# Performance work log

Measured on AMD Instinct MI355X. Metric: run time of the kernel, lower is better.

The kernel has to match this reference:

```python
import jax, jax.numpy as jnp
import numpy as np

B, S, D = 8, 2048, 256
H, HD = 4, 64  # num_heads, head_size; H*HD == D


def setup_inputs() -> dict:
    key = jax.random.key(0)
    ks = jax.random.split(key, 9)
    scale = 0.02
    return {
        "x": jax.random.normal(ks[0], (B, S, D), dtype=jnp.float32),
        "Wq": jax.random.normal(ks[1], (D, H * HD), dtype=jnp.float32) * scale,
        "bq": jnp.zeros((H * HD,), dtype=jnp.float32),
        "Wk": jax.random.normal(ks[2], (D, H * HD), dtype=jnp.float32) * scale,
        "bk": jnp.zeros((H * HD,), dtype=jnp.float32),
        "Wv": jax.random.normal(ks[3], (D, H * HD), dtype=jnp.float32) * scale,
        "bv": jnp.zeros((H * HD,), dtype=jnp.float32),
        "Wo": jax.random.normal(ks[4], (H * HD, D), dtype=jnp.float32) * scale,
        "bo": jnp.zeros((D,), dtype=jnp.float32),
    }


def _split_heads(t):
    # [B, S, H*HD] -> [B, H, S, HD]
    b, s, _ = t.shape
    return t.reshape(b, s, H, HD).transpose(0, 2, 1, 3)


def reference(x, Wq, bq, Wk, bk, Wv, bv, Wo, bo):
    q = _split_heads(x @ Wq + bq)
    k = _split_heads(x @ Wk + bk)
    v = _split_heads(x @ Wv + bv)
    scores = jnp.einsum("bhqd,bhkd->bhqk", q, k) / jnp.sqrt(jnp.float32(HD))
    weights = jax.nn.softmax(scores, axis=-1)
    attn = jnp.einsum("bhqk,bhkd->bhqd", weights, v)  # [B, H, S, HD]
    concat = attn.transpose(0, 2, 1, 3).reshape(x.shape[0], -1, H * HD)
    return concat @ Wo + bo
```

## Files before the change

### kernel.cpp

```cpp
#include <hip/hip_runtime.h>
#include <hip/hip_bf16.h>

namespace {

constexpr int B_ = 8, S = 2048, D = 256, H = 4, HD = 64;
constexpr int M = B_ * S;

typedef __attribute__((ext_vector_type(8))) short bf16x8;
typedef __attribute__((ext_vector_type(4))) short bf16x4;
typedef __attribute__((ext_vector_type(4))) float f32x4;
typedef __attribute__((ext_vector_type(16))) float f32x16;
typedef __attribute__((ext_vector_type(4))) unsigned uint4v;

__device__ inline short f2bf(float x) {
  __hip_bfloat16 h = __float2bfloat16(x);
  short s;
  __builtin_memcpy(&s, &h, 2);
  return s;
}

__device__ inline f32x4 mfma16(bf16x8 a, bf16x8 b, f32x4 c) {
  return __builtin_amdgcn_mfma_f32_16x16x32_bf16(a, b, c, 0, 0, 0);
}
__device__ inline f32x16 mfma32(bf16x8 a, bf16x8 b, f32x16 c) {
  return __builtin_amdgcn_mfma_f32_32x32x16_bf16(a, b, c, 0, 0, 0);
}

__device__ inline float exp2a(float x) {
  float r;
  asm("v_exp_f32 %0, %1" : "=v"(r) : "v"(x));
  return r;
}

__device__ inline unsigned cvtpk(float lo, float hi) {
  unsigned r;
  asm("v_cvt_pk_bf16_f32 %0, %1, %2" : "=v"(r) : "v"(lo), "v"(hi));
  return r;
}

__device__ inline bf16x4 pk4(float a, float b, float c, float d) {
  unsigned lo = cvtpk(a, b), hi = cvtpk(c, d);
  uint2 u{lo, hi};
  bf16x4 r;
  __builtin_memcpy(&r, &u, 8);
  return r;
}

__device__ inline bf16x8 ld_cvt8(const float* p) {
  float4 a = *(const float4*)p;
  float4 b = *(const float4*)(p + 4);
  uint4v u = {cvtpk(a.x, a.y), cvtpk(a.z, a.w), cvtpk(b.x, b.y), cvtpk(b.z, b.w)};
  bf16x8 r;
  __builtin_memcpy(&r, &u, 16);
  return r;
}

__global__ __launch_bounds__(256) void prep_w_kernel(
    const float* __restrict__ Wq, const float* __restrict__ Wk,
    const float* __restrict__ Wv, const float* __restrict__ Wo,
    short* __restrict__ WqT, short* __restrict__ WkT,
    short* __restrict__ WvT, short* __restrict__ WoT) {
  const int blk = blockIdx.x, t = threadIdx.x;
  const int wq = blk >> 4, n0 = (blk & 15) * 16;
  const float* W = wq == 0 ? Wq : wq == 1 ? Wk : wq == 2 ? Wv : Wo;
  short* Wt = wq == 0 ? WqT : wq == 1 ? WkT : wq == 2 ? WvT : WoT;
#pragma unroll
  for (int j4 = 0; j4 < 4; ++j4) {
    float4 v = *(const float4*)(W + (size_t)t * 256 + n0 + j4 * 4);
    Wt[(n0 + j4 * 4 + 0) * 256 + t] = f2bf(v.x);
    Wt[(n0 + j4 * 4 + 1) * 256 + t] = f2bf(v.y);
    Wt[(n0 + j4 * 4 + 2) * 256 + t] = f2bf(v.z);
    Wt[(n0 + j4 * 4 + 3) * 256 + t] = f2bf(v.w);
  }
}

__global__ __launch_bounds__(256) void gemm_qkv_kernel(
    const float* __restrict__ x,
    const short* __restrict__ WqT, const short* __restrict__ WkT,
    const short* __restrict__ WvT,
    const float* __restrict__ bq, const float* __restrict__ bk,
    const float* __restrict__ bv,
    short* __restrict__ Qo, short* __restrict__ Ko, short* __restrict__ Vt) {
  const int bx = blockIdx.x;
  const int which = blockIdx.y;
  const short* Wt = which == 0 ? WqT : which == 1 ? WkT : WvT;
  const float* bias = which == 0 ? bq : which == 1 ? bk : bv;

  __shared__ short Xs[2][64 * 32];
  __shared__ short Ws[2][256 * 32];

  const int tid = threadIdx.x;
  const int wid = tid >> 6, lane = tid & 63;
  const int l15 = lane & 15, l4 = lane >> 4;
  const int nt0 = wid * 4;

  const float* xsrc = x + ((size_t)(bx * 64 + (tid >> 2))) * 256 + (tid & 3) * 8;
  const short* wsrc = Wt + ((size_t)(tid >> 2)) * 256 + (tid & 3) * 8;
  short* xdst0 = &Xs[0][tid * 8];
  short* xdst1 = &Xs[1][tid * 8];
  short* wdst0 = &Ws[0][tid * 8];
  short* wdst1 = &Ws[1][tid * 8];

  bf16x8 xr, wr[4];
  xr = ld_cvt8(xsrc);
#pragma unroll
  for (int p = 0; p < 4; ++p) wr[p] = *(const bf16x8*)(wsrc + (size_t)p * 64 * 256);
  *(bf16x8*)xdst0 = xr;
#pragma unroll
  for (int p = 0; p < 4; ++p) *(bf16x8*)(wdst0 + p * 2048) = wr[p];
  __syncthreads();

  f32x4 acc[4][4];
#pragma unroll
  for (int i = 0; i < 4; ++i)
#pragma unroll
    for (int mh = 0; mh < 4; ++mh) acc[i][mh] = f32x4{0.f, 0.f, 0.f, 0.f};

  for (int ks = 0; ks < 8; ++ks) {
    const int cur = ks & 1;
    if (ks < 7) {
      xr = ld_cvt8(xsrc + (ks + 1) * 32);
#pragma unroll
      for (int p = 0; p < 4; ++p)
        wr[p] = *(const bf16x8*)(wsrc + (size_t)p * 64 * 256 + (ks + 1) * 32);
    }
    bf16x8 wf[4], xf[4];
#pragma unroll
    for (int i = 0; i < 4; ++i)
      wf[i] = *(const bf16x8*)&Ws[cur][((nt0 + i) * 16 + l15) * 32 + l4 * 8];
#pragma unroll
    for (int mh = 0; mh < 4; ++mh)
      xf[mh] = *(const bf16x8*)&Xs[cur][(mh * 16 + l15) * 32 + l4 * 8];
    if (which == 2) {
#pragma unroll
      for (int i = 0; i < 4; ++i)
#pragma unroll
        for (int mh = 0; mh < 4; ++mh)
          acc[i][mh] = mfma16(xf[mh], wf[i], acc[i][mh]);
    } else {
#pragma unroll
      for (int i = 0; i < 4; ++i)
#pragma unroll
        for (int mh = 0; mh < 4; ++mh)
          acc[i][mh] = mfma16(wf[i], xf[mh], acc[i][mh]);
    }
    if (ks < 7) {
      short* xd = (cur ? xdst0 : xdst1);
      short* wd = (cur ? wdst0 : wdst1);
      *(bf16x8*)xd = xr;
#pragma unroll
      for (int p = 0; p < 4; ++p) *(bf16x8*)(wd + p * 2048) = wr[p];
    }
    __syncthreads();
  }

  if (which == 2) {
    const int m0 = bx * 64 + l4 * 4;
#pragma unroll
    for (int i = 0; i < 4; ++i) {
      const int n = (nt0 + i) * 16 + l15;
      const float bi = bias[n];
      const int h = n >> 6, d = n & 63;
#pragma unroll
      for (int mh = 0; mh < 4; ++mh) {
        const int m = m0 + mh * 16;
        const int bb = m >> 11, s0 = m & 2047;
        bf16x4 r = pk4(acc[i][mh][0] + bi, acc[i][mh][1] + bi,
                       acc[i][mh][2] + bi, acc[i][mh][3] + bi);
        *(bf16x4*)(Vt + (((size_t)bb * H + h) * HD + d) * S + s0) = r;
      }
    }
  } else {
    const float scale = which == 0 ? 0.18033688011112042f : 1.0f;
    short* outp = which == 0 ? Qo : Ko;
#pragma unroll
    for (int i = 0; i < 4; ++i) {
      const int n0 = (nt0 + i) * 16 + l4 * 4;
      float4 bi = *(const float4*)(bias + n0);
      const int h = n0 >> 6, d0 = n0 & 63;
#pragma unroll
      for (int mh = 0; mh < 4; ++mh) {
        const int m = bx * 64 + mh * 16 + l15;
        const int bb = m >> 11, s = m & 2047;
        bf16x4 r = pk4((acc[i][mh][0] + bi.x) * scale, (acc[i][mh][1] + bi.y) * scale,
                       (acc[i][mh][2] + bi.z) * scale, (acc[i][mh][3] + bi.w) * scale);
        *(bf16x4*)(outp + (((size_t)bb * H + h) * S + s) * HD + d0) = r;
      }
    }
  }
}

__global__ __launch_bounds__(256) void gemm_out_kernel(
    const short* __restrict__ Abf, const short* __restrict__ WoT,
    const float* __restrict__ bo, float* __restrict__ out) {
  const int bx = blockIdx.x;
  __shared__ short Xs[2][64 * 32];
  __shared__ short Ws[2][256 * 32];

  const int tid = threadIdx.x;
  const int wid = tid >> 6, lane = tid & 63;
  const int l15 = lane & 15, l4 = lane >> 4;
  const int nt0 = wid * 4;

  const short* xsrc = Abf + ((size_t)(bx * 64 + (tid >> 2))) * 256 + (tid & 3) * 8;
  const short* wsrc = WoT + ((size_t)(tid >> 2)) * 256 + (tid & 3) * 8;
  short* xdst0 = &Xs[0][tid * 8];
  short* xdst1 = &Xs[1][tid * 8];
  short* wdst0 = &Ws[0][tid * 8];
  short* wdst1 = &Ws[1][tid * 8];

  bf16x8 xr, wr[4];
  xr = *(const bf16x8*)xsrc;
#pragma unroll
  for (int p = 0; p < 4; ++p) wr[p] = *(const bf16x8*)(wsrc + (size_t)p * 64 * 256);
  *(bf16x8*)xdst0 = xr;
#pragma unroll
  for (int p = 0; p < 4; ++p) *(bf16x8*)(wdst0 + p * 2048) = wr[p];
  __syncthreads();

  f32x4 acc[4][4];
#pragma unroll
  for (int i = 0; i < 4; ++i)
#pragma unroll
    for (int mh = 0; mh < 4; ++mh) acc[i][mh] = f32x4{0.f, 0.f, 0.f, 0.f};

  for (int ks = 0; ks < 8; ++ks) {
    const int cur = ks & 1;
    if (ks < 7) {
      xr = *(const bf16x8*)(xsrc + (ks + 1) * 32);
#pragma unroll
      for (int p = 0; p < 4; ++p)
        wr[p] = *(const bf16x8*)(wsrc + (size_t)p * 64 * 256 + (ks + 1) * 32);
    }
    bf16x8 wf[4], xf[4];
#pragma unroll
    for (int i = 0; i < 4; ++i)
      wf[i] = *(const bf16x8*)&Ws[cur][((nt0 + i) * 16 + l15) * 32 + l4 * 8];
#pragma unroll
    for (int mh = 0; mh < 4; ++mh)
      xf[mh] = *(const bf16x8*)&Xs[cur][(mh * 16 + l15) * 32 + l4 * 8];
#pragma unroll
    for (int i = 0; i < 4; ++i)
#pragma unroll
      for (int mh = 0; mh < 4; ++mh)
        acc[i][mh] = mfma16(wf[i], xf[mh], acc[i][mh]);
    if (ks < 7) {
      short* xd = (cur ? xdst0 : xdst1);
      short* wd = (cur ? wdst0 : wdst1);
      *(bf16x8*)xd = xr;
#pragma unroll
      for (int p = 0; p < 4; ++p) *(bf16x8*)(wd + p * 2048) = wr[p];
    }
    __syncthreads();
  }

#pragma unroll
  for (int i = 0; i < 4; ++i) {
    const int n0 = (nt0 + i) * 16 + l4 * 4;
    float4 bi = *(const float4*)(bo + n0);
#pragma unroll
    for (int mh = 0; mh < 4; ++mh) {
      const int m = bx * 64 + mh * 16 + l15;
      float4 r;
      r.x = acc[i][mh][0] + bi.x;
      r.y = acc[i][mh][1] + bi.y;
      r.z = acc[i][mh][2] + bi.z;
      r.w = acc[i][mh][3] + bi.w;
      *(float4*)(out + (size_t)m * 256 + n0) = r;
    }
  }
}

__global__ __launch_bounds__(256) void attn_kernel13(
    const short* __restrict__ Q, const short* __restrict__ K,
    const short* __restrict__ VT, short* __restrict__ Abf) {
  const int lin = blockIdx.x;
  const int bh = lin & 31;
  const int qt = lin >> 5;
  const int tid = threadIdx.x, wid = tid >> 6, lane = tid & 63;
  const int q31 = lane & 31, h = lane >> 5;
  constexpr int NT = S / 64;

  __shared__ short Ks[2][64 * 128];
  __shared__ short Vs[3][64 * 128];

  const short* Kg = K + (size_t)bh * S * HD;
  const short* Vg = VT + (size_t)bh * HD * S;
  const int qrow = qt * 128 + wid * 32;

  const short* Qg = Q + ((size_t)bh * S + qrow + q31) * HD + h * 8;
  bf16x8 qf[4];
#pragma unroll
  for (int ds = 0; ds < 4; ++ds) qf[ds] = *(const bf16x8*)(Qg + ds * 16);

  bf16x8 ones;
#pragma unroll
  for (int i = 0; i < 8; ++i) ones[i] = (short)0x3F80;

  const int srow = tid >> 2;
  const int scol = (tid & 3) * 16;
  const int swz = (srow & 15) * 8;
  const int c0 = scol ^ swz;
  const int c1 = (scol + 8) ^ swz;

  const int fs = (lane & 15) * 8;
  int kcol[4];
#pragma unroll
  for (int ds = 0; ds < 4; ++ds) kcol[ds] = (ds * 16 + h * 8) ^ fs;

  bf16x8 kr0, kr1, vr0, vr1;
  kr0 = *(const bf16x8*)(Kg + (size_t)srow * HD + scol);
  kr1 = *(const bf16x8*)(Kg + (size_t)srow * HD + scol + 8);
  *(bf16x8*)&Ks[0][srow * 128 + c0] = kr0;
  *(bf16x8*)&Ks[0][srow * 128 + c1] = kr1;
  {
    const short* Kn = Kg + (size_t)64 * HD;
    kr0 = *(const bf16x8*)(Kn + (size_t)srow * HD + scol);
    kr1 = *(const bf16x8*)(Kn + (size_t)srow * HD + scol + 8);
    vr0 = *(const bf16x8*)(Vg + (size_t)srow * S + scol);
    vr1 = *(const bf16x8*)(Vg + (size_t)srow * S + scol + 8);
  }
  __syncthreads();

  f32x16 o0, o1, lsum;
#pragma unroll
  for (int i = 0; i < 16; ++i) { o0[i] = 0.f; o1[i] = 0.f; lsum[i] = 0.f; }
  bf16x8 pB[4];

#define EXPPACK(S0, S1)                                               \
  {                                                                   \
    _Pragma("unroll") for (int win = 0; win < 2; ++win) {             \
      const f32x16& sc = win ? (S1) : (S0);                           \
      float p[16];                                                    \
      _Pragma("unroll") for (int r = 0; r < 16; ++r)                  \
          p[r] = exp2a(sc[r]);                                        \
      unsigned w[8];                                                  \
      _Pragma("unroll") for (int i = 0; i < 8; ++i)                   \
          w[i] = cvtpk(p[2 * i], p[2 * i + 1]);                       \
      unsigned x0 = w[0], y0 = w[2], x1 = w[1], y1 = w[3];            \
      unsigned x2 = w[4], y2 = w[6], x3 = w[5], y3 = w[7];            \
      asm("v_permlane32_swap_b32 %0, %1" : "+v"(x0), "+v"(y0));       \
      asm("v_permlane32_swap_b32 %0, %1" : "+v"(x1), "+v"(y1));       \
      asm("v_permlane32_swap_b32 %0, %1" : "+v"(x2), "+v"(y2));       \
      asm("v_permlane32_swap_b32 %0, %1" : "+v"(x3), "+v"(y3));       \
      uint4v u0 = {x0, x1, y0, y1};                                   \
      uint4v u1 = {x2, x3, y2, y3};                                   \
      __builtin_memcpy(&pB[win * 2 + 0], &u0, 16);                    \
      __builtin_memcpy(&pB[win * 2 + 1], &u1, 16);                    \
    }                                                                 \
  }

  {
    f32x16 sc0, sc1;
#pragma unroll
    for (int i = 0; i < 16; ++i) { sc0[i] = 0.f; sc1[i] = 0.f; }
    __builtin_amdgcn_s_setprio(1);
#pragma unroll
    for (int ds = 0; ds < 4; ++ds) {
      bf16x8 k0 = *(const bf16x8*)&Ks[0][(q31)*128 + kcol[ds]];
      bf16x8 k1 = *(const bf16x8*)&Ks[0][(32 + q31) * 128 + kcol[ds]];
      sc0 = mfma32(k0, qf[ds], sc0);
      sc1 = mfma32(k1, qf[ds], sc1);
    }
    __builtin_amdgcn_s_setprio(0);
    EXPPACK(sc0, sc1);
    *(bf16x8*)&Ks[1][srow * 128 + c0] = kr0;
    *(bf16x8*)&Ks[1][srow * 128 + c1] = kr1;
    *(bf16x8*)&Vs[0][srow * 128 + c0] = vr0;
    *(bf16x8*)&Vs[0][srow * 128 + c1] = vr1;
    __syncthreads();
  }

  int vrd = 0;
  int vwr = 1;
  for (int kt = 1; kt < NT; ++kt) {
    if (kt + 1 < NT) {
      const short* Kn = Kg + (size_t)(kt + 1) * 64 * HD;
      kr0 = *(const bf16x8*)(Kn + (size_t)srow * HD + scol);
      kr1 = *(const bf16x8*)(Kn + (size_t)srow * HD + scol + 8);
    }
    vr0 = *(const bf16x8*)(Vg + (size_t)srow * S + kt * 64 + scol);
    vr1 = *(const bf16x8*)(Vg + (size_t)srow * S + kt * 64 + scol + 8);

    f32x16 sc0, sc1;
#pragma unroll
    for (int i = 0; i < 16; ++i) { sc0[i] = 0.f; sc1[i] = 0.f; }

    const short* kb = &Ks[kt & 1][0];
    const short* vb = &Vs[vrd][0];
    __builtin_amdgcn_s_setprio(1);
#pragma unroll
    for (int ds = 0; ds < 4; ++ds) {
      bf16x8 k0 = *(const bf16x8*)&kb[(q31)*128 + kcol[ds]];
      bf16x8 k1 = *(const bf16x8*)&kb[(32 + q31) * 128 + kcol[ds]];
      sc0 = mfma32(k0, qf[ds], sc0);
      sc1 = mfma32(k1, qf[ds], sc1);
      bf16x8 v0 = *(const bf16x8*)&vb[(q31)*128 + kcol[ds]];
      bf16x8 v1 = *(const bf16x8*)&vb[(32 + q31) * 128 + kcol[ds]];
      o0 = mfma32(v0, pB[ds], o0);
      o1 = mfma32(v1, pB[ds], o1);
      lsum = mfma32(ones, pB[ds], lsum);
    }
    __builtin_amdgcn_s_setprio(0);

    EXPPACK(sc0, sc1);

    if (kt + 1 < NT) {
      short* kw = &Ks[(kt + 1) & 1][0];
      *(bf16x8*)&kw[srow * 128 + c0] = kr0;
      *(bf16x8*)&kw[srow * 128 + c1] = kr1;
    }
    {
      short* vw = &Vs[vwr][0];
      *(bf16x8*)&vw[srow * 128 + c0] = vr0;
      *(bf16x8*)&vw[srow * 128 + c1] = vr1;
    }
    __syncthreads();

    vrd = vwr;
    vwr = (vwr == 2) ? 0 : vwr + 1;
  }

  {
    const short* vb = &Vs[vrd][0];
    __builtin_amdgcn_s_setprio(1);
#pragma unroll
    for (int ds = 0; ds < 4; ++ds) {
      bf16x8 v0 = *(const bf16x8*)&vb[(q31)*128 + kcol[ds]];
      bf16x8 v1 = *(const bf16x8*)&vb[(32 + q31) * 128 + kcol[ds]];
      o0 = mfma32(v0, pB[ds], o0);
      o1 = mfma32(v1, pB[ds], o1);
      lsum = mfma32(ones, pB[ds], lsum);
    }
    __builtin_amdgcn_s_setprio(0);
  }
#undef EXPPACK

  const float inv = 1.0f / lsum[0];
  const int b = bh >> 2, hh = bh & 3;
  short* ap = Abf + ((size_t)b * S + qrow + q31) * 256 + hh * 64;
#pragma unroll
  for (int dt = 0; dt < 2; ++dt) {
    const f32x16& o = dt ? o1 : o0;
#pragma unroll
    for (int g = 0; g < 4; ++g) {
      const int d0 = dt * 32 + 8 * g + 4 * h;
      bf16x4 r = pk4(o[4 * g + 0] * inv, o[4 * g + 1] * inv,
                     o[4 * g + 2] * inv, o[4 * g + 3] * inv);
      *(bf16x4*)(ap + d0) = r;
    }
  }
}

}

extern "C" void kernel_launch(void* const* d_in, const int* in_sizes, int n_in,
                              void* d_out, int out_size, void* d_ws, size_t ws_size,
                              hipStream_t stream) {
  const float* x  = (const float*)d_in[0];
  const float* Wq = (const float*)d_in[1];
  const float* bq = (const float*)d_in[2];
  const float* Wk = (const float*)d_in[3];
  const float* bk = (const float*)d_in[4];
  const float* Wv = (const float*)d_in[5];
  const float* bv = (const float*)d_in[6];
  const float* Wo = (const float*)d_in[7];
  const float* bo = (const float*)d_in[8];
  float* out = (float*)d_out;

  const size_t per = (size_t)M * D;
  short* WqT = (short*)d_ws;
  short* WkT = WqT + 256 * 256;
  short* WvT = WkT + 256 * 256;
  short* WoT = WvT + 256 * 256;
  short* Qbf = WoT + 256 * 256;
  short* Kbf = Qbf + per;
  short* Vt  = Kbf + per;
  short* Abf = Vt + per;

  prep_w_kernel<<<64, 256, 0, stream>>>(Wq, Wk, Wv, Wo, WqT, WkT, WvT, WoT);
  gemm_qkv_kernel<<<dim3(256, 3), 256, 0, stream>>>(x, WqT, WkT, WvT, bq, bk, bv,
                                                    Qbf, Kbf, Vt);
  attn_kernel13<<<512, 256, 0, stream>>>(Qbf, Kbf, Vt, Abf);
  gemm_out_kernel<<<256, 256, 0, stream>>>(Abf, WoT, bo, out);
}
```

Baseline: 88.48 us.

## Software-pipeline attention so QK^T of next tile overlaps exp of previous

Restructures the attention main loop to compute the next tile's QK^T scores into one pair of accumulators while the exponentials and packing of the previous tile's scores run from another pair. The loop is unrolled by two with ping-pong accumulator sets, and the final exp is moved into the epilogue. The aim is to hide the exp/convert latency behind independent MFMA work and cut stalls from the serial dependency. It raises register pressure because of the extra 32 live floats of scores per lane, which risks spills or lower occupancy.

```diff
diff --git a/kernel.cpp b/kernel.cpp
--- a/kernel.cpp
+++ b/kernel.cpp
@@ -271,7 +271,7 @@
   }
 }
 
-__global__ __launch_bounds__(256) void attn_kernel13(
+__global__ __launch_bounds__(256) void attn_kernel14(
     const short* __restrict__ Q, const short* __restrict__ K,
     const short* __restrict__ VT, short* __restrict__ Abf) {
   const int lin = blockIdx.x;
@@ -322,7 +322,7 @@
   }
   __syncthreads();
 
-  f32x16 o0, o1, lsum;
+  f32x16 o0, o1, lsum, scA0, scA1, scB0, scB1;
 #pragma unroll
   for (int i = 0; i < 16; ++i) { o0[i] = 0.f; o1[i] = 0.f; lsum[i] = 0.f; }
   bf16x8 pB[4];
@@ -351,19 +351,17 @@
   }
 
   {
-    f32x16 sc0, sc1;
-#pragma unroll
-    for (int i = 0; i < 16; ++i) { sc0[i] = 0.f; sc1[i] = 0.f; }
+#pragma unroll
+    for (int i = 0; i < 16; ++i) { scA0[i] = 0.f; scA1[i] = 0.f; }
     __builtin_amdgcn_s_setprio(1);
 #pragma unroll
     for (int ds = 0; ds < 4; ++ds) {
       bf16x8 k0 = *(const bf16x8*)&Ks[0][(q31)*128 + kcol[ds]];
       bf16x8 k1 = *(const bf16x8*)&Ks[0][(32 + q31) * 128 + kcol[ds]];
-      sc0 = mfma32(k0, qf[ds], sc0);
-      sc1 = mfma32(k1, qf[ds], sc1);
+      scA0 = mfma32(k0, qf[ds], scA0);
+      scA1 = mfma32(k1, qf[ds], scA1);
     }
     __builtin_amdgcn_s_setprio(0);
-    EXPPACK(sc0, sc1);
     *(bf16x8*)&Ks[1][srow * 128 + c0] = kr0;
     *(bf16x8*)&Ks[1][srow * 128 + c1] = kr1;
     *(bf16x8*)&Vs[0][srow * 128 + c0] = vr0;
@@ -373,55 +371,65 @@
 
   int vrd = 0;
   int vwr = 1;
-  for (int kt = 1; kt < NT; ++kt) {
-    if (kt + 1 < NT) {
-      const short* Kn = Kg + (size_t)(kt + 1) * 64 * HD;
-      kr0 = *(const bf16x8*)(Kn + (size_t)srow * HD + scol);
-      kr1 = *(const bf16x8*)(Kn + (size_t)srow * HD + scol + 8);
-    }
-    vr0 = *(const bf16x8*)(Vg + (size_t)srow * S + kt * 64 + scol);
-    vr1 = *(const bf16x8*)(Vg + (size_t)srow * S + kt * 64 + scol + 8);
-
-    f32x16 sc0, sc1;
-#pragma unroll
-    for (int i = 0; i < 16; ++i) { sc0[i] = 0.f; sc1[i] = 0.f; }
-
-    const short* kb = &Ks[kt & 1][0];
-    const short* vb = &Vs[vrd][0];
-    __builtin_amdgcn_s_setprio(1);
-#pragma unroll
-    for (int ds = 0; ds < 4; ++ds) {
-      bf16x8 k0 = *(const bf16x8*)&kb[(q31)*128 + kcol[ds]];
-      bf16x8 k1 = *(const bf16x8*)&kb[(32 + q31) * 128 + kcol[ds]];
-      sc0 = mfma32(k0, qf[ds], sc0);
-      sc1 = mfma32(k1, qf[ds], sc1);
-      bf16x8 v0 = *(const bf16x8*)&vb[(q31)*128 + kcol[ds]];
-      bf16x8 v1 = *(const bf16x8*)&vb[(32 + q31) * 128 + kcol[ds]];
-      o0 = mfma32(v0, pB[ds], o0);
-      o1 = mfma32(v1, pB[ds], o1);
-      lsum = mfma32(ones, pB[ds], lsum);
-    }
-    __builtin_amdgcn_s_setprio(0);
-
-    EXPPACK(sc0, sc1);
-
-    if (kt + 1 < NT) {
-      short* kw = &Ks[(kt + 1) & 1][0];
-      *(bf16x8*)&kw[srow * 128 + c0] = kr0;
-      *(bf16x8*)&kw[srow * 128 + c1] = kr1;
-    }
-    {
-      short* vw = &Vs[vwr][0];
-      *(bf16x8*)&vw[srow * 128 + c0] = vr0;
-      *(bf16x8*)&vw[srow * 128 + c1] = vr1;
-    }
-    __syncthreads();
-
-    vrd = vwr;
-    vwr = (vwr == 2) ? 0 : vwr + 1;
-  }
+
+#define STEP(KT, SCP0, SCP1, SCN0, SCN1)                                   \
+  {                                                                        \
+    if ((KT) + 1 < NT) {                                                   \
+      const short* Kn = Kg + (size_t)((KT) + 1) * 64 * HD;                 \
+      kr0 = *(const bf16x8*)(Kn + (size_t)srow * HD + scol);               \
+      kr1 = *(const bf16x8*)(Kn + (size_t)srow * HD + scol + 8);           \
+    }                                                                      \
+    vr0 = *(const bf16x8*)(Vg + (size_t)srow * S + (KT) * 64 + scol);      \
+    vr1 = *(const bf16x8*)(Vg + (size_t)srow * S + (KT) * 64 + scol + 8);  \
+    _Pragma("unroll") for (int i = 0; i < 16; ++i) {                       \
+      SCN0[i] = 0.f;                                                       \
+      SCN1[i] = 0.f;                                                       \
+    }                                                                      \
+    {                                                                      \
+      const short* kb = &Ks[(KT)&1][0];                                    \
+      _Pragma("unroll") for (int ds = 0; ds < 4; ++ds) {                   \
+        bf16x8 k0 = *(const bf16x8*)&kb[(q31)*128 + kcol[ds]];             \
+        bf16x8 k1 = *(const bf16x8*)&kb[(32 + q31) * 128 + kcol[ds]];      \
+        SCN0 = mfma32(k0, qf[ds], SCN0);                                   \
+        SCN1 = mfma32(k1, qf[ds], SCN1);                                   \
+      }                                                                    \
+    }                                                                      \
+    EXPPACK(SCP0, SCP1);                                                   \
+    {                                                                      \
+      const short* vb = &Vs[vrd][0];                                       \
+      __builtin_amdgcn_s_setprio(1);                                       \
+      _Pragma("unroll") for (int ds = 0; ds < 4; ++ds) {                   \
+        bf16x8 v0 = *(const bf16x8*)&vb[(q31)*128 + kcol[ds]];             \
+        bf16x8 v1 = *(const bf16x8*)&vb[(32 + q31) * 128 + kcol[ds]];      \
+        o0 = mfma32(v0, pB[ds], o0);                                       \
+        o1 = mfma32(v1, pB[ds], o1);                                       \
+        lsum = mfma32(ones, pB[ds], lsum);                                 \
+      }                                                                    \
+      __builtin_amdgcn_s_setprio(0);                                       \
+    }                                                                      \
+    if ((KT) + 1 < NT) {                                                   \
+      short* kw = &Ks[((KT) + 1) & 1][0];                                  \
+      *(bf16x8*)&kw[srow * 128 + c0] = kr0;                                \
+      *(bf16x8*)&kw[srow * 128 + c1] = kr1;                                \
+    }                                                                      \
+    {                                                                      \
+      short* vw = &Vs[vwr][0];                                             \
+      *(bf16x8*)&vw[srow * 128 + c0] = vr0;                                \
+      *(bf16x8*)&vw[srow * 128 + c1] = vr1;                                \
+    }                                                                      \
+    __syncthreads();                                                       \
+    vrd = vwr;                                                             \
+    vwr = (vwr == 2) ? 0 : vwr + 1;                                        \
+  }
+
+  for (int kt = 1; kt < NT - 1; kt += 2) {
+    STEP(kt, scA0, scA1, scB0, scB1);
+    STEP(kt + 1, scB0, scB1, scA0, scA1);
+  }
+  STEP(NT - 1, scA0, scA1, scB0, scB1);
 
   {
+    EXPPACK(scB0, scB1);
     const short* vb = &Vs[vrd][0];
     __builtin_amdgcn_s_setprio(1);
 #pragma unroll
@@ -434,6 +442,7 @@
     }
     __builtin_amdgcn_s_setprio(0);
   }
+#undef STEP
 #undef EXPPACK
 
   const float inv = 1.0f / lsum[0];
@@ -481,6 +490,6 @@
   prep_w_kernel<<<64, 256, 0, stream>>>(Wq, Wk, Wv, Wo, WqT, WkT, WvT, WoT);
   gemm_qkv_kernel<<<dim3(256, 3), 256, 0, stream>>>(x, WqT, WkT, WvT, bq, bk, bv,
                                                     Qbf, Kbf, Vt);
-  attn_kernel13<<<512, 256, 0, stream>>>(Qbf, Kbf, Vt, Abf);
+  attn_kernel14<<<512, 256, 0, stream>>>(Qbf, Kbf, Vt, Abf);
   gemm_out_kernel<<<256, 256, 0, stream>>>(Abf, WoT, bo, out);
 }
```

Result: faster. 83.56 us (-5.6%).

## Deepen attention software pipeline with two-tile score lookahead and compact LDS layout

Applied to the files above, without the earlier changes.

Restructures the attention main loop so the QK scores for tile kt are computed while the PV product uses probabilities from tile kt-2, with the exp/pack of tile kt-1 in between. The loop is unrolled by two and ping-pongs score and probability registers. The K/V shared-memory tiles are repacked from 64 rows × 128 shorts into 32 rows × 128 shorts, storing two 32-row halves side by side with a new swizzle, which halves LDS footprint. The aim is to hide exp latency behind MFMA work and allow higher occupancy. The cost is more live registers, and the prologue/epilogue buffer indexing has to stay correct.

```diff
diff --git a/kernel.cpp b/kernel.cpp
--- a/kernel.cpp
+++ b/kernel.cpp
@@ -271,7 +271,7 @@
   }
 }
 
-__global__ __launch_bounds__(256) void attn_kernel13(
+__global__ __launch_bounds__(256) void attn_kernel15(
     const short* __restrict__ Q, const short* __restrict__ K,
     const short* __restrict__ VT, short* __restrict__ Abf) {
   const int lin = blockIdx.x;
@@ -281,8 +281,8 @@
   const int q31 = lane & 31, h = lane >> 5;
   constexpr int NT = S / 64;
 
-  __shared__ short Ks[2][64 * 128];
-  __shared__ short Vs[3][64 * 128];
+  __shared__ short Ks[2][32 * 128];
+  __shared__ short Vs[3][32 * 128];
 
   const short* Kg = K + (size_t)bh * S * HD;
   const short* Vg = VT + (size_t)bh * HD * S;
@@ -298,21 +298,28 @@
   for (int i = 0; i < 8; ++i) ones[i] = (short)0x3F80;
 
   const int srow = tid >> 2;
+  const int pr = srow & 31;
   const int scol = (tid & 3) * 16;
-  const int swz = (srow & 15) * 8;
-  const int c0 = scol ^ swz;
-  const int c1 = (scol + 8) ^ swz;
-
-  const int fs = (lane & 15) * 8;
-  int kcol[4];
-#pragma unroll
-  for (int ds = 0; ds < 4; ++ds) kcol[ds] = (ds * 16 + h * 8) ^ fs;
+  const int cb0 = ((srow >> 5) << 6) + scol;
+  const int swz = (pr & 15) * 8;
+  const int c0 = cb0 ^ swz;
+  const int c1 = (cb0 + 8) ^ swz;
+  const int sbase = pr * 128;
+
+  const int fs = (q31 & 15) * 8;
+  int colA[4], colB[4];
+#pragma unroll
+  for (int ds = 0; ds < 4; ++ds) {
+    colA[ds] = (ds * 16 + h * 8) ^ fs;
+    colB[ds] = (64 + ds * 16 + h * 8) ^ fs;
+  }
+  const int rbase = q31 * 128;
 
   bf16x8 kr0, kr1, vr0, vr1;
   kr0 = *(const bf16x8*)(Kg + (size_t)srow * HD + scol);
   kr1 = *(const bf16x8*)(Kg + (size_t)srow * HD + scol + 8);
-  *(bf16x8*)&Ks[0][srow * 128 + c0] = kr0;
-  *(bf16x8*)&Ks[0][srow * 128 + c1] = kr1;
+  *(bf16x8*)&Ks[0][sbase + c0] = kr0;
+  *(bf16x8*)&Ks[0][sbase + c1] = kr1;
   {
     const short* Kn = Kg + (size_t)64 * HD;
     kr0 = *(const bf16x8*)(Kn + (size_t)srow * HD + scol);
@@ -322,12 +329,12 @@
   }
   __syncthreads();
 
-  f32x16 o0, o1, lsum;
+  f32x16 o0, o1, lsum, scA0, scA1, scB0, scB1;
 #pragma unroll
   for (int i = 0; i < 16; ++i) { o0[i] = 0.f; o1[i] = 0.f; lsum[i] = 0.f; }
-  bf16x8 pB[4];
-
-#define EXPPACK(S0, S1)                                               \
+  bf16x8 pBA[4], pBB[4];
+
+#define EXPPACK(S0, S1, PB)                                           \
   {                                                                   \
     _Pragma("unroll") for (int win = 0; win < 2; ++win) {             \
       const f32x16& sc = win ? (S1) : (S0);                           \
@@ -345,95 +352,116 @@
       asm("v_permlane32_swap_b32 %0, %1" : "+v"(x3), "+v"(y3));       \
       uint4v u0 = {x0, x1, y0, y1};                                   \
       uint4v u1 = {x2, x3, y2, y3};                                   \
-      __builtin_memcpy(&pB[win * 2 + 0], &u0, 16);                    \
-      __builtin_memcpy(&pB[win * 2 + 1], &u1, 16);                    \
+      __builtin_memcpy(&PB[win * 2 + 0], &u0, 16);                    \
+      __builtin_memcpy(&PB[win * 2 + 1], &u1, 16);                    \
     }                                                                 \
   }
 
+#define QKBURST(KB, SCN0, SCN1)                                       \
+  {                                                                   \
+    _Pragma("unroll") for (int i = 0; i < 16; ++i) {                  \
+      SCN0[i] = 0.f;                                                  \
+      SCN1[i] = 0.f;                                                  \
+    }                                                                 \
+    const short* kb_ = (KB);                                          \
+    _Pragma("unroll") for (int ds = 0; ds < 4; ++ds) {                \
+      bf16x8 k0 = *(const bf16x8*)&kb_[rbase + colA[ds]];             \
+      bf16x8 k1 = *(const bf16x8*)&kb_[rbase + colB[ds]];             \
+      SCN0 = mfma32(k0, qf[ds], SCN0);                                \
+      SCN1 = mfma32(k1, qf[ds], SCN1);                                \
+    }                                                                 \
+  }
+
+#define PVBURST(VB, PB)                                               \
+  {                                                                   \
+    const short* vb_ = (VB);                                          \
+    _Pragma("unroll") for (int ds = 0; ds < 4; ++ds) {                \
+      bf16x8 v0 = *(const bf16x8*)&vb_[rbase + colA[ds]];             \
+      bf16x8 v1 = *(const bf16x8*)&vb_[rbase + colB[ds]];             \
+      o0 = mfma32(v0, PB[ds], o0);                                    \
+      o1 = mfma32(v1, PB[ds], o1);                                    \
+      lsum = mfma32(ones, PB[ds], lsum);                              \
+    }                                                                 \
+  }
+
+#define STAGEWR(KT)                                                   \
+  {                                                                   \
+    if ((KT) + 1 < NT) {                                              \
+      short* kw = &Ks[((KT) + 1) & 1][0];                             \
+      *(bf16x8*)&kw[sbase + c0] = kr0;                                \
+      *(bf16x8*)&kw[sbase + c1] = kr1;                                \
+    }                                                                 \
+    short* vw_ = &Vs[vw][0];                                          \
+    *(bf16x8*)&vw_[sbase + c0] = vr0;                                 \
+    *(bf16x8*)&vw_[sbase + c1] = vr1;                                 \
+  }
+
+#define LOADS(KT)                                                          \
+  {                                                                        \
+    if ((KT) + 1 < NT) {                                                   \
+      const short* Kn = Kg + (size_t)((KT) + 1) * 64 * HD;                 \
+      kr0 = *(const bf16x8*)(Kn + (size_t)srow * HD + scol);               \
+      kr1 = *(const bf16x8*)(Kn + (size_t)srow * HD + scol + 8);           \
+    }                                                                      \
+    vr0 = *(const bf16x8*)(Vg + (size_t)srow * S + (KT) * 64 + scol);      \
+    vr1 = *(const bf16x8*)(Vg + (size_t)srow * S + (KT) * 64 + scol + 8);  \
+  }
+
+  int vw = 0;
+
   {
-    f32x16 sc0, sc1;
-#pragma unroll
-    for (int i = 0; i < 16; ++i) { sc0[i] = 0.f; sc1[i] = 0.f; }
     __builtin_amdgcn_s_setprio(1);
-#pragma unroll
-    for (int ds = 0; ds < 4; ++ds) {
-      bf16x8 k0 = *(const bf16x8*)&Ks[0][(q31)*128 + kcol[ds]];
-      bf16x8 k1 = *(const bf16x8*)&Ks[0][(32 + q31) * 128 + kcol[ds]];
-      sc0 = mfma32(k0, qf[ds], sc0);
-      sc1 = mfma32(k1, qf[ds], sc1);
-    }
+    QKBURST(&Ks[0][0], scA0, scA1);
     __builtin_amdgcn_s_setprio(0);
-    EXPPACK(sc0, sc1);
-    *(bf16x8*)&Ks[1][srow * 128 + c0] = kr0;
-    *(bf16x8*)&Ks[1][srow * 128 + c1] = kr1;
-    *(bf16x8*)&Vs[0][srow * 128 + c0] = vr0;
-    *(bf16x8*)&Vs[0][srow * 128 + c1] = vr1;
+    STAGEWR(0);
     __syncthreads();
-  }
-
-  int vrd = 0;
-  int vwr = 1;
-  for (int kt = 1; kt < NT; ++kt) {
-    if (kt + 1 < NT) {
-      const short* Kn = Kg + (size_t)(kt + 1) * 64 * HD;
-      kr0 = *(const bf16x8*)(Kn + (size_t)srow * HD + scol);
-      kr1 = *(const bf16x8*)(Kn + (size_t)srow * HD + scol + 8);
-    }
-    vr0 = *(const bf16x8*)(Vg + (size_t)srow * S + kt * 64 + scol);
-    vr1 = *(const bf16x8*)(Vg + (size_t)srow * S + kt * 64 + scol + 8);
-
-    f32x16 sc0, sc1;
-#pragma unroll
-    for (int i = 0; i < 16; ++i) { sc0[i] = 0.f; sc1[i] = 0.f; }
-
-    const short* kb = &Ks[kt & 1][0];
-    const short* vb = &Vs[vrd][0];
+    vw = 1;
+  }
+
+  {
+    LOADS(1);
     __builtin_amdgcn_s_setprio(1);
-#pragma unroll
-    for (int ds = 0; ds < 4; ++ds) {
-      bf16x8 k0 = *(const bf16x8*)&kb[(q31)*128 + kcol[ds]];
-      bf16x8 k1 = *(const bf16x8*)&kb[(32 + q31) * 128 + kcol[ds]];
-      sc0 = mfma32(k0, qf[ds], sc0);
-      sc1 = mfma32(k1, qf[ds], sc1);
-      bf16x8 v0 = *(const bf16x8*)&vb[(q31)*128 + kcol[ds]];
-      bf16x8 v1 = *(const bf16x8*)&vb[(32 + q31) * 128 + kcol[ds]];
-      o0 = mfma32(v0, pB[ds], o0);
-      o1 = mfma32(v1, pB[ds], o1);
-      lsum = mfma32(ones, pB[ds], lsum);
-    }
+    QKBURST(&Ks[1][0], scB0, scB1);
     __builtin_amdgcn_s_setprio(0);
-
-    EXPPACK(sc0, sc1);
-
-    if (kt + 1 < NT) {
-      short* kw = &Ks[(kt + 1) & 1][0];
-      *(bf16x8*)&kw[srow * 128 + c0] = kr0;
-      *(bf16x8*)&kw[srow * 128 + c1] = kr1;
-    }
-    {
-      short* vw = &Vs[vwr][0];
-      *(bf16x8*)&vw[srow * 128 + c0] = vr0;
-      *(bf16x8*)&vw[srow * 128 + c1] = vr1;
-    }
+    EXPPACK(scA0, scA1, pBA);
+    STAGEWR(1);
     __syncthreads();
-
-    vrd = vwr;
-    vwr = (vwr == 2) ? 0 : vwr + 1;
+    vw = 2;
+  }
+
+#define STEP(KT, SCN0, SCN1, SCP0, SCP1, PBN, PBO)                    \
+  {                                                                   \
+    LOADS(KT);                                                        \
+    const int vr2 = (vw + 1 == 3) ? 0 : vw + 1;          \
+    __builtin_amdgcn_s_setprio(1);                                    \
+    QKBURST(&Ks[(KT)&1][0], SCN0, SCN1);                              \
+    PVBURST(&Vs[vr2][0], PBO);                                        \
+    __builtin_amdgcn_s_setprio(0);                                    \
+    EXPPACK(SCP0, SCP1, PBN);                                         \
+    STAGEWR(KT);                                                      \
+    __syncthreads();                                                  \
+    vw = (vw == 2) ? 0 : vw + 1;                                      \
+  }
+
+  for (int kt = 2; kt < NT; kt += 2) {
+    STEP(kt, scA0, scA1, scB0, scB1, pBB, pBA);
+    STEP(kt + 1, scB0, scB1, scA0, scA1, pBA, pBB);
   }
 
   {
-    const short* vb = &Vs[vrd][0];
     __builtin_amdgcn_s_setprio(1);
-#pragma unroll
-    for (int ds = 0; ds < 4; ++ds) {
-      bf16x8 v0 = *(const bf16x8*)&vb[(q31)*128 + kcol[ds]];
-      bf16x8 v1 = *(const bf16x8*)&vb[(32 + q31) * 128 + kcol[ds]];
-      o0 = mfma32(v0, pB[ds], o0);
-      o1 = mfma32(v1, pB[ds], o1);
-      lsum = mfma32(ones, pB[ds], lsum);
-    }
+    PVBURST(&Vs[0][0], pBA);
     __builtin_amdgcn_s_setprio(0);
-  }
+    EXPPACK(scB0, scB1, pBB);
+    __builtin_amdgcn_s_setprio(1);
+    PVBURST(&Vs[1][0], pBB);
+    __builtin_amdgcn_s_setprio(0);
+  }
+#undef STEP
+#undef LOADS
+#undef STAGEWR
+#undef PVBURST
+#undef QKBURST
 #undef EXPPACK
 
   const float inv = 1.0f / lsum[0];
@@ -481,6 +509,6 @@
   prep_w_kernel<<<64, 256, 0, stream>>>(Wq, Wk, Wv, Wo, WqT, WkT, WvT, WoT);
   gemm_qkv_kernel<<<dim3(256, 3), 256, 0, stream>>>(x, WqT, WkT, WvT, bq, bk, bv,
                                                     Qbf, Kbf, Vt);
-  attn_kernel13<<<512, 256, 0, stream>>>(Qbf, Kbf, Vt, Abf);
+  attn_kernel15<<<512, 256, 0, stream>>>(Qbf, Kbf, Vt, Abf);
   gemm_out_kernel<<<256, 256, 0, stream>>>(Abf, WoT, bo, out);
 }
```

New measurement: 83.01 us, median of 3. 1.07x faster.
